# Optimization experiments

Hardware: AMD Instinct MI355X
Metric: run time of the kernel (lower is better)

## Reference

```python
import jax, jax.numpy as jnp
import numpy as np

B, N, D, H, L, DEG = 8, 4096, 128, 4, 3, 16
C = D // H          # per-head out channels = 32
F = 4 * D           # feedforward hidden = 512
E = B * N * DEG     # 524288 edges, block-diagonal per batch


def setup_inputs() -> dict:
    rng = np.random.default_rng(0)
    # Each flattened node receives DEG incoming edges from random sources in the SAME batch block,
    # mirroring the per-batch nonzero(adj) + offset construction in the torch module.
    tgt = np.repeat(np.arange(B * N, dtype=np.int32), DEG)
    block = (np.arange(B * N, dtype=np.int32) // N).repeat(DEG) * N
    src = rng.integers(0, N, size=E, dtype=np.int32) + block
    edge_index = jnp.asarray(np.stack([src, tgt]), dtype=jnp.int32)

    key = jax.random.key(0)
    ks = jax.random.split(key, 16)
    s = 0.05
    inp = {
        "x": jax.random.normal(ks[0], (B, N, D), jnp.float32),
        "lin_l_w": jax.random.normal(ks[1], (L, D, D), jnp.float32) * s,
        "lin_l_b": jnp.zeros((L, D), jnp.float32),
        "lin_r_w": jax.random.normal(ks[2], (L, D, D), jnp.float32) * s,
        "lin_r_b": jnp.zeros((L, D), jnp.float32),
        "att": jax.random.normal(ks[3], (L, H, C), jnp.float32) * s,
        "gat_bias": jnp.zeros((L, D), jnp.float32),
        "ln1_g": jnp.ones((L, D), jnp.float32),
        "ln1_b": jnp.zeros((L, D), jnp.float32),
        "ff1_w": jax.random.normal(ks[4], (L, D, F), jnp.float32) * s,
        "ff1_b": jnp.zeros((L, F), jnp.float32),
        "ff2_w": jax.random.normal(ks[5], (L, F, D), jnp.float32) * s,
        "ff2_b": jnp.zeros((L, D), jnp.float32),
        "ln2_g": jnp.ones((L, D), jnp.float32),
        "ln2_b": jnp.zeros((L, D), jnp.float32),
        "edge_index": edge_index,
    }
    return inp


def _layer_norm(x, g, b):
    mu = jnp.mean(x, axis=-1, keepdims=True)
    var = jnp.mean((x - mu) ** 2, axis=-1, keepdims=True)
    return (x - mu) * jax.lax.rsqrt(var + 1e-5) * g + b


def _gatv2(xf, src, tgt, Wl, bl, Wr, br, att, bias, nseg):
    # xf: [nseg, D] flattened nodes. GATv2Conv (PyG), add_self_loops=False, concat=True, eval mode.
    gl = (xf @ Wl + bl).reshape(nseg, H, C)   # source transform (x_j)
    gr = (xf @ Wr + br).reshape(nseg, H, C)   # target transform (x_i)
    e = jax.nn.leaky_relu(gl[src] + gr[tgt], negative_slope=0.2)   # [E, H, C]
    logits = jnp.einsum('ehc,hc->eh', e, att)                      # [E, H]
    m = jax.ops.segment_max(logits, tgt, num_segments=nseg)        # softmax over incoming edges
    a = jnp.exp(logits - m[tgt])
    den = jax.ops.segment_sum(a, tgt, num_segments=nseg)
    alpha = a / den[tgt]                                           # [E, H]
    msg = gl[src] * alpha[..., None]                               # [E, H, C]
    out = jax.ops.segment_sum(msg, tgt, num_segments=nseg)         # [nseg, H, C]
    return out.reshape(nseg, H * C) + bias


def reference(x, lin_l_w, lin_l_b, lin_r_w, lin_r_b, att, gat_bias,
              ln1_g, ln1_b, ff1_w, ff1_b, ff2_w, ff2_b, ln2_g, ln2_b,
              edge_index):
    b, n, d = x.shape
    nseg = b * n
    src, tgt = edge_index[0], edge_index[1]
    for l in range(lin_l_w.shape[0]):
        xf = _gatv2(x.reshape(nseg, d), src, tgt,
                    lin_l_w[l], lin_l_b[l], lin_r_w[l], lin_r_b[l],
                    att[l], gat_bias[l], nseg)
        x = xf.reshape(b, n, d)
        h = _layer_norm(x, ln1_g[l], ln1_b[l])
        h = jax.nn.silu(h @ ff1_w[l] + ff1_b[l]) @ ff2_w[l] + ff2_b[l]
        x = _layer_norm(x + h, ln2_g[l], ln2_b[l])
    return x
```

## Files before the change

kernel.cpp:

```cpp
#include <hip/hip_runtime.h>
#include <math.h>

#define BB   8
#define NN   4096
#define DD   128
#define HH   4
#define CC   32
#define LLAY 3
#define DEG  16
#define NSEG (BB*NN)
#define FF   512

typedef __bf16 bf16;
typedef __bf16 bf16x4 __attribute__((ext_vector_type(4)));
typedef __bf16 bf16x8 __attribute__((ext_vector_type(8)));
typedef float  f32x4  __attribute__((ext_vector_type(4)));

template<int ACT, typename OutT>
__global__ __launch_bounds__(256) void mfma_gemm(
    const bf16* __restrict__ A, const bf16* __restrict__ Bt,
    const float* __restrict__ bias, OutT* __restrict__ C,
    int M, int N, int K)
{
    __shared__ bf16 As[128 * 32];
    __shared__ bf16 Bs[128 * 32];

    const int tid  = threadIdx.x;
    const int wave = tid >> 6;
    const int lane = tid & 63;
    const int wr   = wave >> 1;
    const int wc   = wave & 1;
    const int bm   = blockIdx.x * 128;
    const int bn   = blockIdx.y * 128;

    const int lr   = lane & 15;
    const int lkp  = ((lane >> 4) ^ (lane & 3)) * 8;

    const int srow = lane >> 2;
    const int skb  = ((lane & 3) ^ ((lane >> 2) & 3)) * 8;

    f32x4 acc[4][4] = {};

    for (int k0 = 0; k0 < K; k0 += 32) {
        #pragma unroll
        for (int r = 0; r < 2; ++r) {
            int chunk = wave * 2 + r;
            const bf16* ga = A + (size_t)(bm + chunk * 16 + srow) * K + k0 + skb;
            __builtin_amdgcn_global_load_lds(
                (const __attribute__((address_space(1))) void*)ga,
                (__attribute__((address_space(3))) void*)(As + chunk * 512),
                16, 0, 0);
            const bf16* gb = Bt + (size_t)(bn + chunk * 16 + srow) * K + k0 + skb;
            __builtin_amdgcn_global_load_lds(
                (const __attribute__((address_space(1))) void*)gb,
                (__attribute__((address_space(3))) void*)(Bs + chunk * 512),
                16, 0, 0);
        }
        __syncthreads();

        bf16x8 af[4], bfr[4];
        #pragma unroll
        for (int i = 0; i < 4; ++i)
            af[i] = *(const bf16x8*)&As[(wr * 64 + i * 16 + lr) * 32 + lkp];
        #pragma unroll
        for (int j = 0; j < 4; ++j)
            bfr[j] = *(const bf16x8*)&Bs[(wc * 64 + j * 16 + lr) * 32 + lkp];
        #pragma unroll
        for (int i = 0; i < 4; ++i)
            #pragma unroll
            for (int j = 0; j < 4; ++j)
                acc[i][j] = __builtin_amdgcn_mfma_f32_16x16x32_bf16(
                    af[i], bfr[j], acc[i][j], 0, 0, 0);
        __syncthreads();
    }

    const int orow = (lane >> 4) * 4;
    #pragma unroll
    for (int j = 0; j < 4; ++j) {
        int gcol = bn + wc * 64 + j * 16 + lr;
        float bv = bias[gcol];
        #pragma unroll
        for (int i = 0; i < 4; ++i) {
            int grow0 = bm + wr * 64 + i * 16 + orow;
            #pragma unroll
            for (int q = 0; q < 4; ++q) {
                float t = acc[i][j][q] + bv;
                if (ACT == 1) t = t / (1.0f + __expf(-t));
                C[(size_t)(grow0 + q) * N + gcol] = (OutT)t;
            }
        }
    }
}

__global__ __launch_bounds__(256) void cvt_weights(
    const float* __restrict__ ll_w, const float* __restrict__ ll_b,
    const float* __restrict__ lr_w, const float* __restrict__ lr_b,
    const float* __restrict__ ff1_w, const float* __restrict__ ff2_w,
    bf16* __restrict__ wlr, bf16* __restrict__ wt1, bf16* __restrict__ wt2,
    float* __restrict__ blr)
{
    int idx = blockIdx.x * 256 + threadIdx.x;
    if (idx < 98304) {
        int l = idx / 32768, e = idx % 32768;
        int n = e >> 7, k = e & 127;
        float v = (n < 128) ? ll_w[l * 16384 + k * 128 + n]
                            : lr_w[l * 16384 + k * 128 + (n - 128)];
        wlr[idx] = (bf16)v;
    } else if (idx < 294912) {
        int r = idx - 98304;
        int l = r >> 16, e = r & 65535;
        int k = e >> 9, n = e & 511;
        wt1[l * 65536 + n * 128 + k] = (bf16)ff1_w[l * 65536 + k * 512 + n];
    } else if (idx < 491520) {
        int r = idx - 294912;
        int l = r >> 16, e = r & 65535;
        int k = e >> 7, n = e & 127;
        wt2[l * 65536 + n * 512 + k] = (bf16)ff2_w[l * 65536 + k * 128 + n];
    } else if (idx < 492288) {
        int r = idx - 491520;
        int l = r / 256, n = r % 256;
        blr[r] = (n < 128) ? ll_b[l * 128 + n] : lr_b[l * 128 + (n - 128)];
    }
}

__global__ __launch_bounds__(256) void cvt_x(
    const float* __restrict__ x, bf16* __restrict__ xb)
{
    int i = (blockIdx.x * 256 + threadIdx.x) * 4;
    float4 v = *(const float4*)(x + i);
    bf16x4 o = { (bf16)v.x, (bf16)v.y, (bf16)v.z, (bf16)v.w };
    *(bf16x4*)(xb + i) = o;
}

__global__ __launch_bounds__(256) void gat_ln_kernel(
    const float* __restrict__ glr,
    const int* __restrict__ src, const float* __restrict__ att,
    const float* __restrict__ bias,
    const float* __restrict__ ln_g, const float* __restrict__ ln_b,
    float* __restrict__ xg, bf16* __restrict__ ln_out)
{
    const int wave = threadIdx.x >> 6;
    const int lane = threadIdx.x & 63;
    const int bid  = blockIdx.x;
    const int sb   = ((bid & 7) << 10) | (bid >> 3);
    const int node = sb * 4 + wave;
    const int c0   = lane * 2;
    const int h    = lane >> 4;

    const float2 gri = *(const float2*)(glr + (size_t)node * 256 + 128 + c0);
    const float a0 = att[h * CC + (c0 & 31)];
    const float a1 = att[h * CC + ((c0 + 1) & 31)];

    float glx[DEG], gly[DEG], logit[DEG];
    const int* sp = src + node * DEG;

    #pragma unroll
    for (int e = 0; e < DEG; ++e) {
        int s = sp[e];
        float2 g = *(const float2*)(glr + (size_t)s * 256 + c0);
        glx[e] = g.x; gly[e] = g.y;
        float v0 = g.x + gri.x; v0 = v0 > 0.0f ? v0 : 0.2f * v0;
        float v1 = g.y + gri.y; v1 = v1 > 0.0f ? v1 : 0.2f * v1;
        float p = v0 * a0 + v1 * a1;
        p += __shfl_xor(p, 1);
        p += __shfl_xor(p, 2);
        p += __shfl_xor(p, 4);
        p += __shfl_xor(p, 8);
        logit[e] = p;
    }

    float m = logit[0];
    #pragma unroll
    for (int e = 1; e < DEG; ++e) m = fmaxf(m, logit[e]);

    float den = 0.0f, accx = 0.0f, accy = 0.0f;
    #pragma unroll
    for (int e = 0; e < DEG; ++e) {
        float a = __expf(logit[e] - m);
        den += a;
        accx = fmaf(a, glx[e], accx);
        accy = fmaf(a, gly[e], accy);
    }
    float inv = 1.0f / den;
    float2 o;
    o.x = accx * inv + bias[c0];
    o.y = accy * inv + bias[c0 + 1];
    *(float2*)(xg + (size_t)node * DD + c0) = o;

    float s = o.x + o.y;
    #pragma unroll
    for (int mk = 1; mk < 64; mk <<= 1) s += __shfl_xor(s, mk);
    const float mu = s * (1.0f / 128.0f);
    float dx = o.x - mu, dy = o.y - mu;
    float q = dx * dx + dy * dy;
    #pragma unroll
    for (int mk = 1; mk < 64; mk <<= 1) q += __shfl_xor(q, mk);
    const float rs = rsqrtf(q * (1.0f / 128.0f) + 1e-5f);

    ln_out[(size_t)node * DD + c0]     = (bf16)(dx * rs * ln_g[c0]     + ln_b[c0]);
    ln_out[(size_t)node * DD + c0 + 1] = (bf16)(dy * rs * ln_g[c0 + 1] + ln_b[c0 + 1]);
}

template<typename OutT>
__global__ __launch_bounds__(256) void ln_res_kernel(
    const float* __restrict__ x, const float* __restrict__ res,
    const float* __restrict__ g, const float* __restrict__ b,
    OutT* __restrict__ out)
{
    const int wave = threadIdx.x >> 6;
    const int lane = threadIdx.x & 63;
    const int row  = blockIdx.x * 4 + wave;
    const int c0   = lane * 2;

    float2 v = *(const float2*)(x + (size_t)row * DD + c0);
    float2 r = *(const float2*)(res + (size_t)row * DD + c0);
    v.x += r.x; v.y += r.y;

    float s = v.x + v.y;
    #pragma unroll
    for (int mk = 1; mk < 64; mk <<= 1) s += __shfl_xor(s, mk);
    const float mu = s * (1.0f / 128.0f);
    float dx = v.x - mu, dy = v.y - mu;
    float q = dx * dx + dy * dy;
    #pragma unroll
    for (int mk = 1; mk < 64; mk <<= 1) q += __shfl_xor(q, mk);
    const float rs = rsqrtf(q * (1.0f / 128.0f) + 1e-5f);

    out[(size_t)row * DD + c0]     = (OutT)(dx * rs * g[c0]     + b[c0]);
    out[(size_t)row * DD + c0 + 1] = (OutT)(dy * rs * g[c0 + 1] + b[c0 + 1]);
}

extern "C" void kernel_launch(void* const* d_in, const int* in_sizes, int n_in,
                              void* d_out, int out_size, void* d_ws, size_t ws_size,
                              hipStream_t stream)
{
    const float* x        = (const float*)d_in[0];
    const float* lin_l_w  = (const float*)d_in[1];
    const float* lin_l_b  = (const float*)d_in[2];
    const float* lin_r_w  = (const float*)d_in[3];
    const float* lin_r_b  = (const float*)d_in[4];
    const float* att      = (const float*)d_in[5];
    const float* gat_bias = (const float*)d_in[6];
    const float* ln1_g    = (const float*)d_in[7];
    const float* ln1_b    = (const float*)d_in[8];
    const float* ff1_w    = (const float*)d_in[9];
    const float* ff1_b    = (const float*)d_in[10];
    const float* ff2_w    = (const float*)d_in[11];
    const float* ff2_b    = (const float*)d_in[12];
    const float* ln2_g    = (const float*)d_in[13];
    const float* ln2_b    = (const float*)d_in[14];
    const int*   src      = (const int*)d_in[15];

    float* out = (float*)d_out;
    float* ws  = (float*)d_ws;

    const size_t NV = (size_t)NSEG * DD;
    float* GLR  = ws;
    float* XG   = GLR + 2 * NV;
    float* FF2O = XG + NV;
    bf16*  XB   = (bf16*)(FF2O + NV);
    bf16*  LN1B = XB + NV;
    bf16*  HID  = LN1B + NV;
    bf16*  WLR  = HID + (size_t)NSEG * FF;
    bf16*  WT1  = WLR + (size_t)LLAY * 256 * DD;
    bf16*  WT2  = WT1 + (size_t)LLAY * FF * DD;
    float* BLR  = (float*)(WT2 + (size_t)LLAY * DD * FF);

    cvt_weights<<<1923, 256, 0, stream>>>(lin_l_w, lin_l_b, lin_r_w, lin_r_b,
                                          ff1_w, ff2_w, WLR, WT1, WT2, BLR);
    cvt_x<<<4096, 256, 0, stream>>>(x, XB);

    for (int l = 0; l < LLAY; ++l) {
        dim3 gLin(NSEG / 128, 256 / 128);
        mfma_gemm<0, float><<<gLin, 256, 0, stream>>>(XB, WLR + (size_t)l*256*DD,
                                                      BLR + l*256, GLR, NSEG, 256, DD);
        gat_ln_kernel<<<NSEG / 4, 256, 0, stream>>>(GLR, src, att + l*HH*CC,
                                                    gat_bias + l*DD,
                                                    ln1_g + l*DD, ln1_b + l*DD,
                                                    XG, LN1B);
        dim3 gF1(NSEG / 128, FF / 128);
        mfma_gemm<1, bf16><<<gF1, 256, 0, stream>>>(LN1B, WT1 + (size_t)l*FF*DD,
                                                    ff1_b + l*FF, HID, NSEG, FF, DD);
        dim3 gF2(NSEG / 128, DD / 128);
        mfma_gemm<0, float><<<gF2, 256, 0, stream>>>(HID, WT2 + (size_t)l*DD*FF,
                                                     ff2_b + l*DD, FF2O, NSEG, DD, FF);
        if (l == LLAY - 1) {
            ln_res_kernel<float><<<NSEG / 4, 256, 0, stream>>>(
                XG, FF2O, ln2_g + l*DD, ln2_b + l*DD, out);
        } else {
            ln_res_kernel<bf16><<<NSEG / 4, 256, 0, stream>>>(
                XG, FF2O, ln2_g + l*DD, ln2_b + l*DD, XB);
        }
    }
}
```

Before: 381.3 us.

## Fuse FF2 GEMM with residual LayerNorm and merge conversion kernels

Replaces the FF2 GEMM plus separate residual+LayerNorm kernel with one kernel that stages the 128x128 GEMM tile in shared memory and applies bias, residual add and LayerNorm before writing. This removes the fp32 FF2 output round trip through global memory and one launch per layer. It also merges the x and weight conversion kernels into one launch and preloads edge source indices in the GAT kernel. The fused kernel uses 64KB of shared memory per block, which may lower occupancy, and serialises the LayerNorm over 32 rows per wave.

```diff
diff --git a/kernel.cpp b/kernel.cpp
--- a/kernel.cpp
+++ b/kernel.cpp
@@ -35,7 +35,6 @@
 
     const int lr   = lane & 15;
     const int lkp  = ((lane >> 4) ^ (lane & 3)) * 8;
-
     const int srow = lane >> 2;
     const int skb  = ((lane & 3) ^ ((lane >> 2) & 3)) * 8;
 
@@ -92,14 +91,121 @@
     }
 }
 
-__global__ __launch_bounds__(256) void cvt_weights(
+template<typename OutT>
+__global__ __launch_bounds__(256) void ff2_ln_kernel(
+    const bf16* __restrict__ A,
+    const bf16* __restrict__ Bt,
+    const float* __restrict__ bias,
+    const float* __restrict__ resid,
+    const float* __restrict__ g, const float* __restrict__ b,
+    OutT* __restrict__ out)
+{
+    __shared__ float pool[128 * 128];
+    bf16* As = (bf16*)pool;
+    bf16* Bs = (bf16*)(pool + 2048);
+
+    const int tid  = threadIdx.x;
+    const int wave = tid >> 6;
+    const int lane = tid & 63;
+    const int wr   = wave >> 1;
+    const int wc   = wave & 1;
+    const int bm   = blockIdx.x * 128;
+
+    const int lr   = lane & 15;
+    const int lkp  = ((lane >> 4) ^ (lane & 3)) * 8;
+    const int srow = lane >> 2;
+    const int skb  = ((lane & 3) ^ ((lane >> 2) & 3)) * 8;
+
+    f32x4 acc[4][4] = {};
+
+    for (int k0 = 0; k0 < 512; k0 += 32) {
+        #pragma unroll
+        for (int r = 0; r < 2; ++r) {
+            int chunk = wave * 2 + r;
+            const bf16* ga = A + (size_t)(bm + chunk * 16 + srow) * 512 + k0 + skb;
+            __builtin_amdgcn_global_load_lds(
+                (const __attribute__((address_space(1))) void*)ga,
+                (__attribute__((address_space(3))) void*)(As + chunk * 512),
+                16, 0, 0);
+            const bf16* gb = Bt + (size_t)(chunk * 16 + srow) * 512 + k0 + skb;
+            __builtin_amdgcn_global_load_lds(
+                (const __attribute__((address_space(1))) void*)gb,
+                (__attribute__((address_space(3))) void*)(Bs + chunk * 512),
+                16, 0, 0);
+        }
+        __syncthreads();
+
+        bf16x8 af[4], bfr[4];
+        #pragma unroll
+        for (int i = 0; i < 4; ++i)
+            af[i] = *(const bf16x8*)&As[(wr * 64 + i * 16 + lr) * 32 + lkp];
+        #pragma unroll
+        for (int j = 0; j < 4; ++j)
+            bfr[j] = *(const bf16x8*)&Bs[(wc * 64 + j * 16 + lr) * 32 + lkp];
+        #pragma unroll
+        for (int i = 0; i < 4; ++i)
+            #pragma unroll
+            for (int j = 0; j < 4; ++j)
+                acc[i][j] = __builtin_amdgcn_mfma_f32_16x16x32_bf16(
+                    af[i], bfr[j], acc[i][j], 0, 0, 0);
+        __syncthreads();
+    }
+
+    const int orow = (lane >> 4) * 4;
+    #pragma unroll
+    for (int j = 0; j < 4; ++j) {
+        int col = wc * 64 + j * 16 + lr;
+        float bv = bias[col];
+        #pragma unroll
+        for (int i = 0; i < 4; ++i) {
+            int row0 = wr * 64 + i * 16 + orow;
+            #pragma unroll
+            for (int q = 0; q < 4; ++q)
+                pool[(row0 + q) * 128 + col] = acc[i][j][q] + bv;
+        }
+    }
+    __syncthreads();
+
+    const int c0 = lane * 2;
+    for (int it = 0; it < 32; ++it) {
+        int row = wave * 32 + it;
+        float2 v = { pool[row * 128 + c0], pool[row * 128 + c0 + 1] };
+        float2 r = *(const float2*)(resid + (size_t)(bm + row) * DD + c0);
+        v.x += r.x; v.y += r.y;
+
+        float s = v.x + v.y;
+        #pragma unroll
+        for (int mk = 1; mk < 64; mk <<= 1) s += __shfl_xor(s, mk);
+        const float mu = s * (1.0f / 128.0f);
+        float dx = v.x - mu, dy = v.y - mu;
+        float q = dx * dx + dy * dy;
+        #pragma unroll
+        for (int mk = 1; mk < 64; mk <<= 1) q += __shfl_xor(q, mk);
+        const float rs = rsqrtf(q * (1.0f / 128.0f) + 1e-5f);
+
+        out[(size_t)(bm + row) * DD + c0]     = (OutT)(dx * rs * g[c0]     + b[c0]);
+        out[(size_t)(bm + row) * DD + c0 + 1] = (OutT)(dy * rs * g[c0 + 1] + b[c0 + 1]);
+    }
+}
+
+#define CVT_XN  1048576
+__global__ __launch_bounds__(256) void cvt_all(
+    const float* __restrict__ x,
     const float* __restrict__ ll_w, const float* __restrict__ ll_b,
     const float* __restrict__ lr_w, const float* __restrict__ lr_b,
     const float* __restrict__ ff1_w, const float* __restrict__ ff2_w,
-    bf16* __restrict__ wlr, bf16* __restrict__ wt1, bf16* __restrict__ wt2,
-    float* __restrict__ blr)
-{
-    int idx = blockIdx.x * 256 + threadIdx.x;
+    bf16* __restrict__ xb, bf16* __restrict__ wlr,
+    bf16* __restrict__ wt1, bf16* __restrict__ wt2, float* __restrict__ blr)
+{
+    int gid = blockIdx.x * 256 + threadIdx.x;
+    if (gid < CVT_XN) {
+        int i = gid * 4;
+        float4 v = *(const float4*)(x + i);
+        bf16x4 o = { (bf16)v.x, (bf16)v.y, (bf16)v.z, (bf16)v.w };
+        *(bf16x4*)(xb + i) = o;
+        return;
+    }
+    int idx = gid - CVT_XN;
     if (idx < 98304) {
         int l = idx / 32768, e = idx % 32768;
         int n = e >> 7, k = e & 127;
@@ -123,15 +229,6 @@
     }
 }
 
-__global__ __launch_bounds__(256) void cvt_x(
-    const float* __restrict__ x, bf16* __restrict__ xb)
-{
-    int i = (blockIdx.x * 256 + threadIdx.x) * 4;
-    float4 v = *(const float4*)(x + i);
-    bf16x4 o = { (bf16)v.x, (bf16)v.y, (bf16)v.z, (bf16)v.w };
-    *(bf16x4*)(xb + i) = o;
-}
-
 __global__ __launch_bounds__(256) void gat_ln_kernel(
     const float* __restrict__ glr,
     const int* __restrict__ src, const float* __restrict__ att,
@@ -151,16 +248,20 @@
     const float a0 = att[h * CC + (c0 & 31)];
     const float a1 = att[h * CC + ((c0 + 1) & 31)];
 
+    int sidx[DEG];
+    const int* sp = src + node * DEG;
+    #pragma unroll
+    for (int e = 0; e < DEG; ++e) sidx[e] = sp[e];
+
     float glx[DEG], gly[DEG], logit[DEG];
-    const int* sp = src + node * DEG;
 
     #pragma unroll
     for (int e = 0; e < DEG; ++e) {
-        int s = sp[e];
-        float2 g = *(const float2*)(glr + (size_t)s * 256 + c0);
-        glx[e] = g.x; gly[e] = g.y;
-        float v0 = g.x + gri.x; v0 = v0 > 0.0f ? v0 : 0.2f * v0;
-        float v1 = g.y + gri.y; v1 = v1 > 0.0f ? v1 : 0.2f * v1;
+        float2 gv = *(const float2*)(glr + (size_t)sidx[e] * 256 + c0);
+        glx[e] = gv.x; gly[e] = gv.y;
+        float s0 = gv.x + gri.x, s1 = gv.y + gri.y;
+        float v0 = fmaxf(s0, 0.2f * s0);
+        float v1 = fmaxf(s1, 0.2f * s1);
         float p = v0 * a0 + v1 * a1;
         p += __shfl_xor(p, 1);
         p += __shfl_xor(p, 2);
@@ -199,35 +300,6 @@
 
     ln_out[(size_t)node * DD + c0]     = (bf16)(dx * rs * ln_g[c0]     + ln_b[c0]);
     ln_out[(size_t)node * DD + c0 + 1] = (bf16)(dy * rs * ln_g[c0 + 1] + ln_b[c0 + 1]);
-}
-
-template<typename OutT>
-__global__ __launch_bounds__(256) void ln_res_kernel(
-    const float* __restrict__ x, const float* __restrict__ res,
-    const float* __restrict__ g, const float* __restrict__ b,
-    OutT* __restrict__ out)
-{
-    const int wave = threadIdx.x >> 6;
-    const int lane = threadIdx.x & 63;
-    const int row  = blockIdx.x * 4 + wave;
-    const int c0   = lane * 2;
-
-    float2 v = *(const float2*)(x + (size_t)row * DD + c0);
-    float2 r = *(const float2*)(res + (size_t)row * DD + c0);
-    v.x += r.x; v.y += r.y;
-
-    float s = v.x + v.y;
-    #pragma unroll
-    for (int mk = 1; mk < 64; mk <<= 1) s += __shfl_xor(s, mk);
-    const float mu = s * (1.0f / 128.0f);
-    float dx = v.x - mu, dy = v.y - mu;
-    float q = dx * dx + dy * dy;
-    #pragma unroll
-    for (int mk = 1; mk < 64; mk <<= 1) q += __shfl_xor(q, mk);
-    const float rs = rsqrtf(q * (1.0f / 128.0f) + 1e-5f);
-
-    out[(size_t)row * DD + c0]     = (OutT)(dx * rs * g[c0]     + b[c0]);
-    out[(size_t)row * DD + c0 + 1] = (OutT)(dy * rs * g[c0 + 1] + b[c0 + 1]);
 }
 
 extern "C" void kernel_launch(void* const* d_in, const int* in_sizes, int n_in,
@@ -257,8 +329,7 @@
     const size_t NV = (size_t)NSEG * DD;
     float* GLR  = ws;
     float* XG   = GLR + 2 * NV;
-    float* FF2O = XG + NV;
-    bf16*  XB   = (bf16*)(FF2O + NV);
+    bf16*  XB   = (bf16*)(XG + NV);
     bf16*  LN1B = XB + NV;
     bf16*  HID  = LN1B + NV;
     bf16*  WLR  = HID + (size_t)NSEG * FF;
@@ -266,9 +337,8 @@
     bf16*  WT2  = WT1 + (size_t)LLAY * FF * DD;
     float* BLR  = (float*)(WT2 + (size_t)LLAY * DD * FF);
 
-    cvt_weights<<<1923, 256, 0, stream>>>(lin_l_w, lin_l_b, lin_r_w, lin_r_b,
-                                          ff1_w, ff2_w, WLR, WT1, WT2, BLR);
-    cvt_x<<<4096, 256, 0, stream>>>(x, XB);
+    cvt_all<<<6018, 256, 0, stream>>>(x, lin_l_w, lin_l_b, lin_r_w, lin_r_b,
+                                      ff1_w, ff2_w, XB, WLR, WT1, WT2, BLR);
 
     for (int l = 0; l < LLAY; ++l) {
         dim3 gLin(NSEG / 128, 256 / 128);
@@ -281,15 +351,14 @@
         dim3 gF1(NSEG / 128, FF / 128);
         mfma_gemm<1, bf16><<<gF1, 256, 0, stream>>>(LN1B, WT1 + (size_t)l*FF*DD,
                                                     ff1_b + l*FF, HID, NSEG, FF, DD);
-        dim3 gF2(NSEG / 128, DD / 128);
-        mfma_gemm<0, float><<<gF2, 256, 0, stream>>>(HID, WT2 + (size_t)l*DD*FF,
-                                                     ff2_b + l*DD, FF2O, NSEG, DD, FF);
         if (l == LLAY - 1) {
-            ln_res_kernel<float><<<NSEG / 4, 256, 0, stream>>>(
-                XG, FF2O, ln2_g + l*DD, ln2_b + l*DD, out);
+            ff2_ln_kernel<float><<<NSEG / 128, 256, 0, stream>>>(
+                HID, WT2 + (size_t)l*DD*FF, ff2_b + l*DD, XG,
+                ln2_g + l*DD, ln2_b + l*DD, out);
         } else {
-            ln_res_kernel<bf16><<<NSEG / 4, 256, 0, stream>>>(
-                XG, FF2O, ln2_g + l*DD, ln2_b + l*DD, XB);
-        }
-    }
-}
+            ff2_ln_kernel<bf16><<<NSEG / 128, 256, 0, stream>>>(
+                HID, WT2 + (size_t)l*DD*FF, ff2_b + l*DD, XG,
+                ln2_g + l*DD, ln2_b + l*DD, XB);
+        }
+    }
+}
```

Result: slower. 393.6 us (+3.2%).
